# Kernel tuning notes

Measured on AMD Instinct MI355X. Metric: run time of the kernel, lower is better.

The kernel has to match this reference:

```python
import jax, jax.numpy as jnp
import numpy as np

EMB_DIM = 1024
B, T = 32, 2048
N_FLIGHTS = 30
# Action index layout (ActionEnumerator): 0=no_flight, 1=cancel, 2=no_reservation,
# 3..32 = book flight i, 33..62 = change flight i  -> n_actions = 63

def setup_inputs() -> dict:
    key = jax.random.key(0)
    k0, k1, k2, k3, k4 = jax.random.split(key, 5)
    scale = 1.0 / np.sqrt(EMB_DIM)
    return {
        "embs": jax.random.normal(k0, (B, T, EMB_DIM), dtype=jnp.float32),
        "W_status": jax.random.uniform(k1, (5, EMB_DIM), jnp.float32, -scale, scale),
        "b_status": jax.random.uniform(k2, (5,), jnp.float32, -scale, scale),
        "W_flight": jax.random.uniform(k3, (N_FLIGHTS, EMB_DIM), jnp.float32, -scale, scale),
        "b_flight": jax.random.uniform(k4, (N_FLIGHTS,), jnp.float32, -scale, scale),
    }

def reference(embs, W_status, b_status, W_flight, b_flight):
    # Two small linear heads + softmax
    status_probs = jax.nn.softmax(jnp.einsum('bte,se->bts', embs, W_status) + b_status, axis=-1)
    flight_probs = jax.nn.softmax(jnp.einsum('bte,fe->btf', embs, W_flight) + b_flight, axis=-1)
    no_flight = status_probs[:, :, 0:1]
    no_reservation = status_probs[:, :, 1:2]
    cancel = status_probs[:, :, 2:3]
    change = status_probs[:, :, 3:4]
    book = status_probs[:, :, 4:5]
    # Fused version of the 30-iteration scatter loop: one concat of outer products.
    final_probs = jnp.concatenate(
        [no_flight, cancel, no_reservation,
         book * flight_probs,     # [B,T,30] book flight i
         change * flight_probs],  # [B,T,30] change flight i
        axis=-1)  # [B, T, 63]
    return final_probs
```

## Files before the change

### kernel.cpp

```cpp
#include <hip/hip_runtime.h>
#include <math.h>


typedef __bf16 bf16x8 __attribute__((ext_vector_type(8)));
typedef float  f32x4  __attribute__((ext_vector_type(4)));

#define ROWS_PER_BLOCK 256
#define KSTEPS   32
#define HALF_KS  16

__global__ __launch_bounds__(1024, 4)
void fused_heads_kernel(const float* __restrict__ embs,
                        const float* __restrict__ W_status,
                        const float* __restrict__ b_status,
                        const float* __restrict__ W_flight,
                        const float* __restrict__ b_flight,
                        float* __restrict__ out) {
    __shared__ bf16x8 Bsh[HALF_KS * 3 * 64];

    const int tid  = threadIdx.x;
    const int lane = tid & 63;
    const int wv   = tid >> 6;
    const int n    = lane & 15;
    const int q    = lane >> 4;

    const int rowbase = blockIdx.x * ROWS_PER_BLOCK + wv * 16;
    const float* aptr = embs + (size_t)(rowbase + n) * 1024 + q * 8;

    f32x4 acc0 = {0.f, 0.f, 0.f, 0.f};
    f32x4 acc1 = {0.f, 0.f, 0.f, 0.f};
    f32x4 acc2 = {0.f, 0.f, 0.f, 0.f};

    float4 ca0 = *(const float4*)(aptr);
    float4 ca1 = *(const float4*)(aptr + 4);

    for (int half = 0; half < 2; ++half) {
        __syncthreads();

#pragma unroll
        for (int i = 0; i < 3; ++i) {
            const int d   = tid + i * 1024;
            const int L   = d & 63;
            const int ksf = d >> 6;
            const int ksl = ksf / 3;
            const int f   = ksf - ksl * 3;
            const int bn  = f * 16 + (L & 15);
            const int bk  = (half * HALF_KS + ksl) * 32 + (L >> 4) * 8;
            bf16x8 w;
#pragma unroll
            for (int j = 0; j < 8; ++j) w[j] = (__bf16)0.0f;
            if (bn < 35) {
                const float* src = (bn < 5) ? (W_status + bn * 1024 + bk)
                                            : (W_flight + (bn - 5) * 1024 + bk);
                const float4 w0 = *(const float4*)(src);
                const float4 w1 = *(const float4*)(src + 4);
                w[0] = (__bf16)w0.x; w[1] = (__bf16)w0.y;
                w[2] = (__bf16)w0.z; w[3] = (__bf16)w0.w;
                w[4] = (__bf16)w1.x; w[5] = (__bf16)w1.y;
                w[6] = (__bf16)w1.z; w[7] = (__bf16)w1.w;
            }
            Bsh[d] = w;
        }
        __syncthreads();

#pragma unroll 4
        for (int kl = 0; kl < HALF_KS; ++kl) {
            const int ks  = half * HALF_KS + kl;
            const int nks = (ks < KSTEPS - 1) ? ks + 1 : ks;
            const float4 na0 = *(const float4*)(aptr + nks * 32);
            const float4 na1 = *(const float4*)(aptr + nks * 32 + 4);

            bf16x8 af;
            af[0] = (__bf16)ca0.x; af[1] = (__bf16)ca0.y;
            af[2] = (__bf16)ca0.z; af[3] = (__bf16)ca0.w;
            af[4] = (__bf16)ca1.x; af[5] = (__bf16)ca1.y;
            af[6] = (__bf16)ca1.z; af[7] = (__bf16)ca1.w;

            const bf16x8 b0 = Bsh[(kl * 3 + 0) * 64 + lane];
            const bf16x8 b1 = Bsh[(kl * 3 + 1) * 64 + lane];
            const bf16x8 b2 = Bsh[(kl * 3 + 2) * 64 + lane];

            acc0 = __builtin_amdgcn_mfma_f32_16x16x32_bf16(af, b0, acc0, 0, 0, 0);
            acc1 = __builtin_amdgcn_mfma_f32_16x16x32_bf16(af, b1, acc1, 0, 0, 0);
            acc2 = __builtin_amdgcn_mfma_f32_16x16x32_bf16(af, b2, acc2, 0, 0, 0);

            ca0 = na0; ca1 = na1;
        }
    }

    const float bias0 = (n < 5) ? b_status[n] : b_flight[n - 5];
    const float bias1 = b_flight[n + 11];
    const float bias2 = (n < 3) ? b_flight[n + 27] : 0.0f;
    const int   gb    = lane & 48;

#pragma unroll
    for (int i = 0; i < 4; ++i) {
        const float v0 = acc0[i] + bias0;
        const float v1 = acc1[i] + bias1;
        const float v2 = (n < 3) ? (acc2[i] + bias2) : -INFINITY;

        float ms = (n < 5) ? v0 : -INFINITY;
        float mf = fmaxf((n >= 5) ? v0 : -INFINITY, fmaxf(v1, v2));
#pragma unroll
        for (int m = 1; m < 16; m <<= 1) {
            ms = fmaxf(ms, __shfl_xor(ms, m));
            mf = fmaxf(mf, __shfl_xor(mf, m));
        }

        const float es  = (n < 5)  ? __expf(v0 - ms) : 0.0f;
        const float ef0 = (n >= 5) ? __expf(v0 - mf) : 0.0f;
        const float ef1 = __expf(v1 - mf);
        const float ef2 = (n < 3)  ? __expf(v2 - mf) : 0.0f;

        float ss = es;
        float sf = ef0 + ef1 + ef2;
#pragma unroll
        for (int m = 1; m < 16; m <<= 1) {
            ss += __shfl_xor(ss, m);
            sf += __shfl_xor(sf, m);
        }
        const float invs = 1.0f / ss;
        const float invf = 1.0f / sf;

        const float book   = __shfl(es, gb + 4) * invs * invf;
        const float change = __shfl(es, gb + 3) * invs * invf;

        float* orow = out + (size_t)(rowbase + q * 4 + i) * 63;
        if (n == 0) orow[0] = es * invs;
        if (n == 2) orow[1] = es * invs;
        if (n == 1) orow[2] = es * invs;
        if (n >= 5) {
            orow[3 + (n - 5)]  = book   * ef0;
            orow[33 + (n - 5)] = change * ef0;
        }
        orow[3 + (n + 11)]  = book   * ef1;
        orow[33 + (n + 11)] = change * ef1;
        if (n < 3) {
            orow[3 + (n + 27)]  = book   * ef2;
            orow[33 + (n + 27)] = change * ef2;
        }
    }
}

extern "C" void kernel_launch(void* const* d_in, const int* in_sizes, int n_in,
                              void* d_out, int out_size, void* d_ws, size_t ws_size,
                              hipStream_t stream) {
    const float* embs     = (const float*)d_in[0];
    const float* W_status = (const float*)d_in[1];
    const float* b_status = (const float*)d_in[2];
    const float* W_flight = (const float*)d_in[3];
    const float* b_flight = (const float*)d_in[4];
    float* out = (float*)d_out;

    const int rows = in_sizes[0] / 1024;
    const int grid = rows / ROWS_PER_BLOCK;

    fused_heads_kernel<<<grid, 1024, 0, stream>>>(
        embs, W_status, b_status, W_flight, b_flight, out);
}
```

Baseline: 390.8 us.

## Stage embedding tiles through double-buffered swizzled LDS with coalesced row loads

Before this change, each lane read its own 32-byte slice straight from global memory in the MFMA fragment layout. Now the 256-row by 32-column embedding tile is loaded cooperatively, with 8 consecutive threads covering one 128-byte row chunk. The tile goes into a double-buffered, XOR-swizzled LDS array, and the next tile is prefetched two steps ahead. The goal is better-coalesced global reads for this memory-bound GEMV-like kernel, at the cost of 64 KB of extra LDS, which limits occupancy, and a block-wide barrier on every k-step.

Result: no change. 395.9 us (+1.3%).

```diff
diff --git a/kernel.cpp b/kernel.cpp
--- a/kernel.cpp
+++ b/kernel.cpp
@@ -5,9 +5,8 @@
 typedef __bf16 bf16x8 __attribute__((ext_vector_type(8)));
 typedef float  f32x4  __attribute__((ext_vector_type(4)));
 
-#define ROWS_PER_BLOCK 256
-#define KSTEPS   32
-#define HALF_KS  16
+#define KSTEPS  32
+#define HALF_KS 16
 
 __global__ __launch_bounds__(1024, 4)
 void fused_heads_kernel(const float* __restrict__ embs,
@@ -16,6 +15,7 @@
                         const float* __restrict__ W_flight,
                         const float* __restrict__ b_flight,
                         float* __restrict__ out) {
+    __shared__ float4 Atile[2][256 * 8];
     __shared__ bf16x8 Bsh[HALF_KS * 3 * 64];
 
     const int tid  = threadIdx.x;
@@ -23,20 +23,18 @@
     const int wv   = tid >> 6;
     const int n    = lane & 15;
     const int q    = lane >> 4;
+    const int row0 = blockIdx.x * 256;
 
-    const int rowbase = blockIdx.x * ROWS_PER_BLOCK + wv * 16;
-    const float* aptr = embs + (size_t)(rowbase + n) * 1024 + q * 8;
+    const float4* E4 = (const float4*)embs;
 
-    f32x4 acc0 = {0.f, 0.f, 0.f, 0.f};
-    f32x4 acc1 = {0.f, 0.f, 0.f, 0.f};
-    f32x4 acc2 = {0.f, 0.f, 0.f, 0.f};
+    const int srow = tid >> 3;
+    const int sc4  = tid & 7;
+    const int sswz = sc4 ^ (srow & 7);
 
-    float4 ca0 = *(const float4*)(aptr);
-    float4 ca1 = *(const float4*)(aptr + 4);
+    const int abase = (wv * 16 + n) * 8;
+    const int aswz  = n & 7;
 
-    for (int half = 0; half < 2; ++half) {
-        __syncthreads();
-
+    auto stageB = [&](int half) {
 #pragma unroll
         for (int i = 0; i < 3; ++i) {
             const int d   = tid + i * 1024;
@@ -61,20 +59,39 @@
             }
             Bsh[d] = w;
         }
-        __syncthreads();
+    };
 
-#pragma unroll 4
+    f32x4 acc0 = {0.f, 0.f, 0.f, 0.f};
+    f32x4 acc1 = {0.f, 0.f, 0.f, 0.f};
+    f32x4 acc2 = {0.f, 0.f, 0.f, 0.f};
+
+    float4 sr0 = E4[(size_t)(row0 + srow)       * 256 + 0 * 8 + sc4];
+    float4 sr1 = E4[(size_t)(row0 + srow + 128) * 256 + 0 * 8 + sc4];
+    Atile[0][srow * 8 + sswz]         = sr0;
+    Atile[0][(srow + 128) * 8 + sswz] = sr1;
+    sr0 = E4[(size_t)(row0 + srow)       * 256 + 1 * 8 + sc4];
+    sr1 = E4[(size_t)(row0 + srow + 128) * 256 + 1 * 8 + sc4];
+    stageB(0);
+    __syncthreads();
+
+    for (int half = 0; half < 2; ++half) {
+        if (half == 1) {
+            stageB(1);
+            __syncthreads();
+        }
+#pragma unroll
         for (int kl = 0; kl < HALF_KS; ++kl) {
-            const int ks  = half * HALF_KS + kl;
-            const int nks = (ks < KSTEPS - 1) ? ks + 1 : ks;
-            const float4 na0 = *(const float4*)(aptr + nks * 32);
-            const float4 na1 = *(const float4*)(aptr + nks * 32 + 4);
+            const int ks   = half * HALF_KS + kl;
+            const int buf  = kl & 1;
+            const int nbuf = buf ^ 1;
 
+            const float4 a0 = Atile[buf][abase + ((q * 2)     ^ aswz)];
+            const float4 a1 = Atile[buf][abase + ((q * 2 + 1) ^ aswz)];
             bf16x8 af;
-            af[0] = (__bf16)ca0.x; af[1] = (__bf16)ca0.y;
-            af[2] = (__bf16)ca0.z; af[3] = (__bf16)ca0.w;
-            af[4] = (__bf16)ca1.x; af[5] = (__bf16)ca1.y;
-            af[6] = (__bf16)ca1.z; af[7] = (__bf16)ca1.w;
+            af[0] = (__bf16)a0.x; af[1] = (__bf16)a0.y;
+            af[2] = (__bf16)a0.z; af[3] = (__bf16)a0.w;
+            af[4] = (__bf16)a1.x; af[5] = (__bf16)a1.y;
+            af[6] = (__bf16)a1.z; af[7] = (__bf16)a1.w;
 
             const bf16x8 b0 = Bsh[(kl * 3 + 0) * 64 + lane];
             const bf16x8 b1 = Bsh[(kl * 3 + 1) * 64 + lane];
@@ -84,7 +101,14 @@
             acc1 = __builtin_amdgcn_mfma_f32_16x16x32_bf16(af, b1, acc1, 0, 0, 0);
             acc2 = __builtin_amdgcn_mfma_f32_16x16x32_bf16(af, b2, acc2, 0, 0, 0);
 
-            ca0 = na0; ca1 = na1;
+            Atile[nbuf][srow * 8 + sswz]         = sr0;
+            Atile[nbuf][(srow + 128) * 8 + sswz] = sr1;
+
+            const int nt = (ks + 2 < KSTEPS) ? ks + 2 : KSTEPS - 1;
+            sr0 = E4[(size_t)(row0 + srow)       * 256 + nt * 8 + sc4];
+            sr1 = E4[(size_t)(row0 + srow + 128) * 256 + nt * 8 + sc4];
+
+            __syncthreads();
         }
     }
 
@@ -93,6 +117,7 @@
     const float bias2 = (n < 3) ? b_flight[n + 27] : 0.0f;
     const int   gb    = lane & 48;
 
+    const int rowbase = row0 + wv * 16;
 #pragma unroll
     for (int i = 0; i < 4; ++i) {
         const float v0 = acc0[i] + bias0;
@@ -153,7 +178,7 @@
     float* out = (float*)d_out;
 
     const int rows = in_sizes[0] / 1024;
-    const int grid = rows / ROWS_PER_BLOCK;
+    const int grid = rows / 256;
 
     fused_heads_kernel<<<grid, 1024, 0, stream>>>(
         embs, W_status, b_status, W_flight, b_flight, out);
```
